# Optimization experiments

Measured on AMD Instinct MI355X. Metric: run time of the kernel, lower is better.

## Reference

```python
import jax, jax.numpy as jnp
import numpy as np

EPS = 1e-7
IOU_THRESHOLD = 0.5
PENALTY_FACTOR = 0.1
BOX_LOSS_WEIGHT = 5.0
OBJ_LOSS_WEIGHT = 1.0
SMALL_OBJ_SCALE = 2.0
SMALL_SIZE_THRESHOLD = 0.05


def _xywh_to_xyxy(b):
    return jnp.concatenate([b[..., :2] - b[..., 2:] / 2, b[..., :2] + b[..., 2:] / 2], axis=-1)


def _bbox_ciou(box1, box2, eps=EPS):
    # box1, box2: (..., 4) in xyxy format
    b1_x1, b1_y1, b1_x2, b1_y2 = box1[..., 0], box1[..., 1], box1[..., 2], box1[..., 3]
    b2_x1, b2_y1, b2_x2, b2_y2 = box2[..., 0], box2[..., 1], box2[..., 2], box2[..., 3]
    b1_area = (b1_x2 - b1_x1) * (b1_y2 - b1_y1)
    b2_area = (b2_x2 - b2_x1) * (b2_y2 - b2_y1)
    inter_w = jnp.clip(jnp.minimum(b1_x2, b2_x2) - jnp.maximum(b1_x1, b2_x1), 0)
    inter_h = jnp.clip(jnp.minimum(b1_y2, b2_y2) - jnp.maximum(b1_y1, b2_y1), 0)
    inter_area = inter_w * inter_h
    union_area = b1_area + b2_area - inter_area + eps
    iou = inter_area / union_area
    c2 = (jnp.maximum(b1_x2, b2_x2) - jnp.minimum(b1_x1, b2_x1)) ** 2 + \
         (jnp.maximum(b1_y2, b2_y2) - jnp.minimum(b1_y1, b2_y1)) ** 2 + eps
    center_dist2 = ((b1_x1 + b1_x2) / 2 - (b2_x1 + b2_x2) / 2) ** 2 + \
                   ((b1_y1 + b1_y2) / 2 - (b2_y1 + b2_y2) / 2) ** 2
    w1, h1 = b1_x2 - b1_x1, b1_y2 - b1_y1
    w2, h2 = b2_x2 - b2_x1, b2_y2 - b2_y1
    v = (4.0 / (jnp.pi ** 2)) * (jnp.arctan(w1 / (h1 + eps)) - jnp.arctan(w2 / (h2 + eps))) ** 2
    alpha = v / (1 - iou + v + eps)
    return iou - (center_dist2 / c2 + alpha * v)


def setup_inputs() -> dict:
    key = jax.random.key(0)
    k0, k1, k2, k3, k4 = jax.random.split(key, 5)
    B, Np, Ng, C = 16, 8192, 128, 80
    return {
        "batch_y_hat": jax.random.uniform(k0, (B, Np, 4), dtype=jnp.float32),
        "batch_y": jax.random.uniform(k1, (B, Ng, 4), dtype=jnp.float32),
        "batch_obj_scores": jax.random.normal(k2, (B, Np), dtype=jnp.float32),
        "batch_class_pred": jax.random.normal(k3, (B, Np, C), dtype=jnp.float32),
        "batch_class_target": jax.random.randint(k4, (B, Ng), 0, C),
        "min_obj_score": 0,
    }


def reference(batch_y_hat, batch_y, batch_obj_scores, batch_class_pred, batch_class_target, min_obj_score):
    valid = batch_obj_scores > min_obj_score                      # (B, Np) kept predictions
    p = _xywh_to_xyxy(batch_y_hat)                                # (B, Np, 4)
    g = _xywh_to_xyxy(batch_y)                                    # (B, Ng, 4)
    # pairwise IoU (xywh compute_iou, which has no eps)
    lt = jnp.maximum(p[:, :, None, :2], g[:, None, :, :2])       # (B, Np, Ng, 2)
    rb = jnp.minimum(p[:, :, None, 2:], g[:, None, :, 2:])
    wh = jnp.clip(rb - lt, 0)
    inter = wh[..., 0] * wh[..., 1]                               # (B, Np, Ng)
    area_p = (p[..., 2] - p[..., 0]) * (p[..., 3] - p[..., 1])
    area_g = (g[..., 2] - g[..., 0]) * (g[..., 3] - g[..., 1])
    iou_mat = inter / (area_p[:, :, None] + area_g[:, None, :] - inter)
    max_iou = jnp.max(iou_mat, axis=-1)                           # (B, Np)
    match_idx = jnp.argmax(iou_mat, axis=-1)                      # (B, Np)
    matched = valid & (max_iou > IOU_THRESHOLD)
    unmatched = valid & ~matched
    # CIoU localization loss over matched preds
    matched_gt_xyxy = jnp.take_along_axis(g, match_idx[..., None], axis=1)   # (B, Np, 4)
    ciou_loss = 1.0 - _bbox_ciou(p, matched_gt_xyxy)              # (B, Np)
    is_small = (batch_y[..., 2] < SMALL_SIZE_THRESHOLD) | (batch_y[..., 3] < SMALL_SIZE_THRESHOLD)  # (B, Ng)
    w_small = jnp.where(jnp.take_along_axis(is_small, match_idx, axis=1), SMALL_OBJ_SCALE, 1.0)
    n_match = jnp.sum(matched, axis=1)
    loc_loss = jnp.where(n_match > 0,
                         jnp.sum(ciou_loss * w_small * matched, axis=1) / jnp.maximum(n_match, 1),
                         0.0)
    # classification loss over matched preds
    logp = jax.nn.log_softmax(batch_class_pred, axis=-1)          # (B, Np, C)
    tgt = jnp.take_along_axis(batch_class_target, match_idx, axis=1)
    ce = -jnp.take_along_axis(logp, tgt[..., None], axis=-1)[..., 0]
    cls_loss = jnp.where(n_match > 0,
                         jnp.sum(ce * w_small * matched, axis=1) / jnp.maximum(n_match, 1),
                         0.0)
    # penalty on unmatched objectness scores
    penalty = PENALTY_FACTOR * jnp.sum(batch_obj_scores * unmatched, axis=1)
    # objectness BCE-with-logits over valid preds, FN reweighted x2
    s = batch_obj_scores
    lbl = matched.astype(s.dtype)
    bce = jnp.clip(s, 0) - s * lbl + jnp.log1p(jnp.exp(-jnp.abs(s)))
    w_obj = jnp.where(matched & (s < 0.5), 2.0, 1.0)
    n_valid = jnp.sum(valid, axis=1)
    obj_loss = jnp.where(n_valid > 0,
                         jnp.sum(bce * w_obj * valid, axis=1) / jnp.maximum(n_valid, 1),
                         0.0)
    per_batch = BOX_LOSS_WEIGHT * loc_loss + OBJ_LOSS_WEIGHT * obj_loss + penalty + cls_loss
    valid_b = n_valid > 0
    n_vb = jnp.sum(valid_b)
    return jnp.sum(jnp.where(valid_b, per_batch, 0.0)) / jnp.maximum(n_vb, 1)
```

## Files before the change

kernel.cpp:

```cpp
#include <hip/hip_runtime.h>
#include <math.h>

#define B_  16
#define NP_ 8192
#define NG_ 128
#define NC_ 80
#define PPB_ 64
#define NBX_ (NP_ / PPB_)

#define EPS_       1e-7f
#define IOU_THR_   0.5f
#define PEN_       0.1f
#define BOXW_      5.0f
#define SMALLSC_   2.0f
#define SMALLTH_   0.05f


__global__ __launch_bounds__(256) void yolo_main(
    const float* __restrict__ y_hat,
    const float* __restrict__ ygt,
    const float* __restrict__ obj,
    const float* __restrict__ clsp,
    const int*   __restrict__ tgt,
    const int*   __restrict__ min_s,
    float* __restrict__ part)
{
    __shared__ float4 g4[NG_];
    __shared__ float  garea[NG_], gws[NG_];
    __shared__ int    gtc[NG_];
    __shared__ float4 mbuf[3][PPB_];

    const int b   = blockIdx.y;
    const int tid = threadIdx.x;
    const int pl  = tid & 63;
    const int q   = tid >> 6;
    const int p   = blockIdx.x * PPB_ + pl;

    if (tid < NG_) {
        float4 gb = *(const float4*)(ygt + ((size_t)b * NG_ + tid) * 4);
        float x1 = gb.x - gb.z * 0.5f, y1 = gb.y - gb.w * 0.5f;
        float x2 = gb.x + gb.z * 0.5f, y2 = gb.y + gb.w * 0.5f;
        g4[tid] = make_float4(x1, y1, x2, y2);
        garea[tid] = (x2 - x1) * (y2 - y1);
        gws[tid]   = ((gb.z < SMALLTH_) || (gb.w < SMALLTH_)) ? SMALLSC_ : 1.0f;
        gtc[tid]   = tgt[b * NG_ + tid];
    }
    __syncthreads();

    const float min_score = (float)min_s[0];

    float4 pb = *(const float4*)(y_hat + ((size_t)b * NP_ + p) * 4);
    float px1 = pb.x - pb.z * 0.5f, py1 = pb.y - pb.w * 0.5f;
    float px2 = pb.x + pb.z * 0.5f, py2 = pb.y + pb.w * 0.5f;
    float area_p = (px2 - px1) * (py2 - py1);

    float bi_inter = -1.0f, bi_union = 1.0f;
    const int j0 = q * 32;
    int bi = j0;
    #pragma unroll 8
    for (int jj = 0; jj < 32; ++jj) {
        int j = j0 + jj;
        float4 g = g4[j];
        float w = fmaxf(fminf(px2, g.z) - fmaxf(px1, g.x), 0.0f);
        float h = fmaxf(fminf(py2, g.w) - fmaxf(py1, g.y), 0.0f);
        float inter = w * h;
        float uni = area_p + garea[j] - inter;
        bool better = inter * bi_union > bi_inter * uni;
        bi_inter = better ? inter : bi_inter;
        bi_union = better ? uni   : bi_union;
        bi       = better ? j     : bi;
    }

    if (q != 0) mbuf[q - 1][pl] = make_float4(bi_inter, bi_union, (float)bi, 0.f);
    __syncthreads();
    if (q != 0) return;

    #pragma unroll
    for (int k = 0; k < 3; ++k) {
        float4 o = mbuf[k][pl];
        if (o.x * bi_union > bi_inter * o.y) {
            bi_inter = o.x; bi_union = o.y; bi = (int)o.z;
        }
    }
    float max_iou = bi_inter / bi_union;

    float s = obj[(size_t)b * NP_ + p];
    bool valid     = s > min_score;
    bool matched   = valid && (max_iou > IOU_THR_);
    bool unmatched = valid && !matched;

    float f_loc = 0.f, f_ce = 0.f, f_pen = 0.f, f_bce = 0.f;
    float n_m = matched ? 1.f : 0.f;
    float n_v = valid   ? 1.f : 0.f;
    if (unmatched) f_pen = PEN_ * s;

    if (valid) {
        float lbl = matched ? 1.f : 0.f;
        float bce = fmaxf(s, 0.f) - s * lbl + log1pf(expf(-fabsf(s)));
        float w_obj = (matched && s < 0.5f) ? 2.f : 1.f;
        f_bce = bce * w_obj;
    }

    if (matched) {
        float wsm = gws[bi];
        float4 g = g4[bi];
        float bx1 = g.x, by1 = g.y, bx2 = g.z, by2 = g.w;
        float b1a = (px2 - px1) * (py2 - py1);
        float b2a = (bx2 - bx1) * (by2 - by1);
        float iw = fmaxf(fminf(px2, bx2) - fmaxf(px1, bx1), 0.f);
        float ih = fmaxf(fminf(py2, by2) - fmaxf(py1, by1), 0.f);
        float inter = iw * ih;
        float uni = b1a + b2a - inter + EPS_;
        float iou = inter / uni;
        float cw = fmaxf(px2, bx2) - fminf(px1, bx1);
        float ch = fmaxf(py2, by2) - fminf(py1, by1);
        float c2 = cw * cw + ch * ch + EPS_;
        float dx = (px1 + px2) * 0.5f - (bx1 + bx2) * 0.5f;
        float dy = (py1 + py2) * 0.5f - (by1 + by2) * 0.5f;
        float rho2 = dx * dx + dy * dy;
        float w1 = px2 - px1, h1 = py2 - py1;
        float w2 = bx2 - bx1, h2 = by2 - by1;
        float dat = atanf(w1 / (h1 + EPS_)) - atanf(w2 / (h2 + EPS_));
        float v = (float)(4.0 / (M_PI * M_PI)) * dat * dat;
        float alpha = v / (1.f - iou + v + EPS_);
        float ciou = iou - (rho2 / c2 + alpha * v);
        f_loc = (1.f - ciou) * wsm;

        const float* row = clsp + ((size_t)b * NP_ + p) * NC_;
        float m = -INFINITY;
        #pragma unroll
        for (int k = 0; k < NC_ / 4; ++k) {
            float4 v4 = ((const float4*)row)[k];
            m = fmaxf(m, fmaxf(fmaxf(v4.x, v4.y), fmaxf(v4.z, v4.w)));
        }
        float se = 0.f;
        #pragma unroll
        for (int k = 0; k < NC_ / 4; ++k) {
            float4 v4 = ((const float4*)row)[k];
            se += expf(v4.x - m) + expf(v4.y - m) + expf(v4.z - m) + expf(v4.w - m);
        }
        int t = gtc[bi];
        float ce = -(row[t] - m - logf(se));
        f_ce = ce * wsm;
    }

    float vals[6] = { n_m, n_v, f_loc, f_ce, f_pen, f_bce };
    #pragma unroll
    for (int i = 0; i < 6; ++i) {
        float v = vals[i];
        #pragma unroll
        for (int off = 32; off > 0; off >>= 1)
            v += __shfl_down(v, off, 64);
        vals[i] = v;
    }
    if (pl == 0) {
        float* slot = part + ((size_t)b * NBX_ + blockIdx.x) * 6;
        #pragma unroll
        for (int i = 0; i < 6; ++i) slot[i] = vals[i];
    }
}

__global__ __launch_bounds__(64) void yolo_final(const float* __restrict__ part,
                                                 float* __restrict__ out)
{
    int lane = threadIdx.x;
    int b    = lane >> 2;
    int sub  = lane & 3;

    float v[6] = {0.f, 0.f, 0.f, 0.f, 0.f, 0.f};
    for (int k = 0; k < NBX_ / 4; ++k) {
        const float* slot = part + ((size_t)b * NBX_ + sub + 4 * k) * 6;
        #pragma unroll
        for (int i = 0; i < 6; ++i) v[i] += slot[i];
    }
    #pragma unroll
    for (int i = 0; i < 6; ++i) {
        v[i] += __shfl_xor(v[i], 1, 64);
        v[i] += __shfl_xor(v[i], 2, 64);
    }

    float pbv = 0.f, cnt = 0.f;
    if (sub == 0) {
        float nm = v[0], nv = v[1];
        float loc = nm > 0.f ? v[2] / nm : 0.f;
        float ce  = nm > 0.f ? v[3] / nm : 0.f;
        float ob  = nv > 0.f ? v[5] / nv : 0.f;
        float per = BOXW_ * loc + ob + v[4] + ce;
        if (nv > 0.f) { pbv = per; cnt = 1.f; }
    }
    #pragma unroll
    for (int off = 32; off > 0; off >>= 1) {
        pbv += __shfl_down(pbv, off, 64);
        cnt += __shfl_down(cnt, off, 64);
    }
    if (lane == 0) out[0] = pbv / fmaxf(cnt, 1.f);
}

extern "C" void kernel_launch(void* const* d_in, const int* in_sizes, int n_in,
                              void* d_out, int out_size, void* d_ws, size_t ws_size,
                              hipStream_t stream) {
    const float* y_hat = (const float*)d_in[0];
    const float* ygt   = (const float*)d_in[1];
    const float* obj   = (const float*)d_in[2];
    const float* clsp  = (const float*)d_in[3];
    const int*   tgt   = (const int*)d_in[4];
    const int*   mins  = (const int*)d_in[5];
    float* part = (float*)d_ws;
    float* out  = (float*)d_out;

    dim3 grid(NBX_, B_);
    yolo_main<<<grid, 256, 0, stream>>>(y_hat, ygt, obj, clsp, tgt, mins, part);
    yolo_final<<<1, 64, 0, stream>>>(part, out);
}
```

Before: 106.4 us.

## Split softmax cross-entropy over class logits across all four waves

```diff
diff --git a/kernel.cpp b/kernel.cpp
--- a/kernel.cpp
+++ b/kernel.cpp
@@ -7,6 +7,7 @@
 #define NC_ 80
 #define PPB_ 64
 #define NBX_ (NP_ / PPB_)
+#define QCH_ (NC_ / 4)
 
 #define EPS_       1e-7f
 #define IOU_THR_   0.5f
@@ -28,7 +29,10 @@
     __shared__ float4 g4[NG_];
     __shared__ float  garea[NG_], gws[NG_];
     __shared__ int    gtc[NG_];
-    __shared__ float4 mbuf[3][PPB_];
+    __shared__ float4 mbuf[4][PPB_];
+    __shared__ float  cmax[4][PPB_];
+    __shared__ float  csum[4][PPB_];
+    __shared__ float  tlog[PPB_];
 
     const int b   = blockIdx.y;
     const int tid = threadIdx.x;
@@ -71,28 +75,66 @@
         bi       = better ? j     : bi;
     }
 
-    if (q != 0) mbuf[q - 1][pl] = make_float4(bi_inter, bi_union, (float)bi, 0.f);
-    __syncthreads();
+    mbuf[q][pl] = make_float4(bi_inter, bi_union, (float)bi, 0.f);
+    __syncthreads();
+
+    {
+        float4 m0 = mbuf[0][pl];
+        bi_inter = m0.x; bi_union = m0.y; bi = (int)m0.z;
+        #pragma unroll
+        for (int k = 1; k < 4; ++k) {
+            float4 o = mbuf[k][pl];
+            if (o.x * bi_union > bi_inter * o.y) {
+                bi_inter = o.x; bi_union = o.y; bi = (int)o.z;
+            }
+        }
+    }
+    float max_iou = bi_inter / bi_union;
+
+    float s = obj[(size_t)b * NP_ + p];
+    bool valid   = s > min_score;
+    bool matched = valid && (max_iou > IOU_THR_);
+
+    const float* rowq = clsp + ((size_t)b * NP_ + p) * NC_ + q * QCH_;
+    float4 v0, v1, v2, v3, v4;
+    if (matched) {
+        v0 = ((const float4*)rowq)[0];
+        v1 = ((const float4*)rowq)[1];
+        v2 = ((const float4*)rowq)[2];
+        v3 = ((const float4*)rowq)[3];
+        v4 = ((const float4*)rowq)[4];
+        float m = fmaxf(
+            fmaxf(fmaxf(fmaxf(v0.x, v0.y), fmaxf(v0.z, v0.w)),
+                  fmaxf(fmaxf(v1.x, v1.y), fmaxf(v1.z, v1.w))),
+            fmaxf(fmaxf(fmaxf(v2.x, v2.y), fmaxf(v2.z, v2.w)),
+                  fmaxf(fmaxf(fmaxf(v3.x, v3.y), fmaxf(v3.z, v3.w)),
+                        fmaxf(fmaxf(v4.x, v4.y), fmaxf(v4.z, v4.w)))));
+        cmax[q][pl] = m;
+    }
+    __syncthreads();
+
+    float Mall = 0.f;
+    if (matched) {
+        Mall = fmaxf(fmaxf(cmax[0][pl], cmax[1][pl]), fmaxf(cmax[2][pl], cmax[3][pl]));
+        float se = 0.f;
+        se += expf(v0.x - Mall) + expf(v0.y - Mall) + expf(v0.z - Mall) + expf(v0.w - Mall);
+        se += expf(v1.x - Mall) + expf(v1.y - Mall) + expf(v1.z - Mall) + expf(v1.w - Mall);
+        se += expf(v2.x - Mall) + expf(v2.y - Mall) + expf(v2.z - Mall) + expf(v2.w - Mall);
+        se += expf(v3.x - Mall) + expf(v3.y - Mall) + expf(v3.z - Mall) + expf(v3.w - Mall);
+        se += expf(v4.x - Mall) + expf(v4.y - Mall) + expf(v4.z - Mall) + expf(v4.w - Mall);
+        csum[q][pl] = se;
+        int t = gtc[bi];
+        if (t / QCH_ == q)
+            tlog[pl] = rowq[t - q * QCH_];
+    }
+    __syncthreads();
+
     if (q != 0) return;
-
-    #pragma unroll
-    for (int k = 0; k < 3; ++k) {
-        float4 o = mbuf[k][pl];
-        if (o.x * bi_union > bi_inter * o.y) {
-            bi_inter = o.x; bi_union = o.y; bi = (int)o.z;
-        }
-    }
-    float max_iou = bi_inter / bi_union;
-
-    float s = obj[(size_t)b * NP_ + p];
-    bool valid     = s > min_score;
-    bool matched   = valid && (max_iou > IOU_THR_);
-    bool unmatched = valid && !matched;
 
     float f_loc = 0.f, f_ce = 0.f, f_pen = 0.f, f_bce = 0.f;
     float n_m = matched ? 1.f : 0.f;
     float n_v = valid   ? 1.f : 0.f;
-    if (unmatched) f_pen = PEN_ * s;
+    if (valid && !matched) f_pen = PEN_ * s;
 
     if (valid) {
         float lbl = matched ? 1.f : 0.f;
@@ -126,21 +168,8 @@
         float ciou = iou - (rho2 / c2 + alpha * v);
         f_loc = (1.f - ciou) * wsm;
 
-        const float* row = clsp + ((size_t)b * NP_ + p) * NC_;
-        float m = -INFINITY;
-        #pragma unroll
-        for (int k = 0; k < NC_ / 4; ++k) {
-            float4 v4 = ((const float4*)row)[k];
-            m = fmaxf(m, fmaxf(fmaxf(v4.x, v4.y), fmaxf(v4.z, v4.w)));
-        }
-        float se = 0.f;
-        #pragma unroll
-        for (int k = 0; k < NC_ / 4; ++k) {
-            float4 v4 = ((const float4*)row)[k];
-            se += expf(v4.x - m) + expf(v4.y - m) + expf(v4.z - m) + expf(v4.w - m);
-        }
-        int t = gtc[bi];
-        float ce = -(row[t] - m - logf(se));
+        float se = ((csum[0][pl] + csum[1][pl]) + csum[2][pl]) + csum[3][pl];
+        float ce = -(tlog[pl] - Mall - logf(se));
         f_ce = ce * wsm;
     }
 
@@ -154,9 +183,9 @@
         vals[i] = v;
     }
     if (pl == 0) {
-        float* slot = part + ((size_t)b * NBX_ + blockIdx.x) * 6;
-        #pragma unroll
-        for (int i = 0; i < 6; ++i) slot[i] = vals[i];
+        float4* slot = (float4*)(part + ((size_t)b * NBX_ + blockIdx.x) * 8);
+        slot[0] = make_float4(vals[0], vals[1], vals[2], vals[3]);
+        slot[1] = make_float4(vals[4], vals[5], 0.f, 0.f);
     }
 }
 
@@ -169,9 +198,11 @@
 
     float v[6] = {0.f, 0.f, 0.f, 0.f, 0.f, 0.f};
     for (int k = 0; k < NBX_ / 4; ++k) {
-        const float* slot = part + ((size_t)b * NBX_ + sub + 4 * k) * 6;
-        #pragma unroll
-        for (int i = 0; i < 6; ++i) v[i] += slot[i];
+        const float4* slot = (const float4*)(part + ((size_t)b * NBX_ + sub + 4 * k) * 8);
+        float4 a = slot[0];
+        float4 c = slot[1];
+        v[0] += a.x; v[1] += a.y; v[2] += a.z; v[3] += a.w;
+        v[4] += c.x; v[5] += c.y;
     }
     #pragma unroll
     for (int i = 0; i < 6; ++i) {
```

Result: no change. 105.0 us (-1.3%).
